# Performance work log

Hardware: AMD Instinct MI355X
Metric: run time of the kernel (lower is better)

The kernel has to match this reference:

```python
import jax, jax.numpy as jnp
import numpy as np

NEG_INF = -1e9  # stands in for the -inf diagonal mask of criss-cross attention
BN_EPS = 1e-5


def conv1x1(x, w, b=None):
    # x: [B,Cin,H,W], w: [Cout,Cin]
    y = jnp.einsum('bchw,oc->bohw', x, w)
    if b is not None:
        y = y + b[None, :, None, None]
    return y


def criss_cross(qf, kf, vf, q_w, q_b, k_w, k_b, v_w, v_b, gamma):
    # Criss-cross attention (CCNet): row + column affinity, joint softmax, aggregate.
    B, C, H, W = vf.shape
    q = conv1x1(qf, q_w, q_b)  # [B,Ci,H,W]
    k = conv1x1(kf, k_w, k_b)  # [B,Ci,H,W]
    v = conv1x1(vf, v_w, v_b)  # [B,C,H,W]
    # column-wise (along H) energy, with -inf on the self position (h == h')
    eH = jnp.einsum('bchw,bcHw->bhwH', q, k)
    eH = eH + NEG_INF * jnp.eye(H, dtype=eH.dtype)[:, None, :]  # [H,1,H] broadcasts over w
    # row-wise (along W) energy
    eW = jnp.einsum('bchw,bchW->bhwW', q, k)
    att = jax.nn.softmax(jnp.concatenate([eH, eW], axis=-1), axis=-1)  # [B,H,W,H+W]
    aH, aW = att[..., :H], att[..., H:]
    outH = jnp.einsum('bcHw,bhwH->bchw', v, aH)
    outW = jnp.einsum('bchW,bhwW->bchw', v, aW)
    return gamma * (outH + outW) + vf


def batchnorm(x, scale, bias):
    # training-mode BN over (N,H,W)
    mean = x.mean(axis=(0, 2, 3), keepdims=True)
    var = x.var(axis=(0, 2, 3), keepdims=True)
    xh = (x - mean) * jax.lax.rsqrt(var + BN_EPS)
    return xh * scale[None, :, None, None] + bias[None, :, None, None]


def setup_inputs() -> dict:
    key = jax.random.key(0)
    ks = jax.random.split(key, 16)
    B, C, H, W = 8, 512, 96, 96
    Hh, Wh = 48, 48
    Cin = C // 2    # 256
    Ci = C // 16    # 32
    s = 0.02
    inp = {
        'low_feature': jax.random.normal(ks[0], (B, C, H, W), jnp.float32),
        'high_feature': jax.random.normal(ks[1], (B, C, Hh, Wh), jnp.float32),
        'conv1_w': jax.random.normal(ks[2], (Cin, C), jnp.float32) * s,
        'conv1_b': jnp.zeros((Cin,), jnp.float32),
        'conv2_w': jax.random.normal(ks[3], (Cin, C), jnp.float32) * s,
        'conv2_b': jnp.zeros((Cin,), jnp.float32),
        'q_w': jax.random.normal(ks[4], (Ci, Cin), jnp.float32) * s,
        'q_b': jnp.zeros((Ci,), jnp.float32),
        'k_w': jax.random.normal(ks[5], (Ci, Cin), jnp.float32) * s,
        'k_b': jnp.zeros((Ci,), jnp.float32),
        'v_w': jax.random.normal(ks[6], (Cin, Cin), jnp.float32) * s,
        'v_b': jnp.zeros((Cin,), jnp.float32),
        'gamma': jnp.array(0.1, jnp.float32),
        'bottleneck_w': jax.random.normal(ks[7], (C, Cin + C), jnp.float32) * s,
        'bn_scale': jnp.ones((C,), jnp.float32),
        'bn_bias': jnp.zeros((C,), jnp.float32),
    }
    return inp


def reference(low_feature, high_feature, conv1_w, conv1_b, conv2_w, conv2_b,
              q_w, q_b, k_w, k_b, v_w, v_b, gamma, bottleneck_w, bn_scale, bn_bias):
    B, C, H, W = low_feature.shape
    hf = jax.image.resize(high_feature, (B, high_feature.shape[1], H, W), method='bilinear')
    qf = conv1x1(low_feature, conv1_w, conv1_b)   # [B,C/2,H,W]
    vf = conv1x1(hf, conv2_w, conv2_b)            # [B,C/2,H,W]
    for _ in range(2):  # module applies the same attention twice
        vf = criss_cross(qf, vf, vf, q_w, q_b, k_w, k_b, v_w, v_b, gamma)
    cat = jnp.concatenate([vf, hf], axis=1)       # [B, C/2 + C, H, W]
    out = conv1x1(cat, bottleneck_w)              # bias=False
    out = batchnorm(out, bn_scale, bn_bias)
    return jax.nn.relu(out)
```

## Files before the change

kernel.cpp:

```cpp
#include <hip/hip_runtime.h>
#include <hip/hip_bf16.h>

typedef __hip_bfloat16 bf16;
typedef __attribute__((ext_vector_type(8))) short short8;
typedef __attribute__((ext_vector_type(4))) float f32x4;

constexpr int kHW = 96 * 96;

__device__ __forceinline__ float b2f(bf16 x){ return __bfloat162float(x); }
__device__ __forceinline__ bf16  f2b(float x){ return __float2bfloat16(x); }
__device__ __forceinline__ unsigned short b2u(bf16 x){ return *(unsigned short*)&x; }

#define SW(r, g) ((r)*32 + ((((g) ^ (((r) >> 1) & 3))) << 3))


__global__ void k_zero(float* __restrict__ p){
  int i = blockIdx.x*256 + threadIdx.x;
  if (i < 1024) p[i] = 0.0f;
}

__global__ void k_cvt(const float* __restrict__ s, bf16* __restrict__ d, int n){
  int i = blockIdx.x*256 + threadIdx.x;
  if (i < n) d[i] = f2b(s[i]);
}

__global__ __launch_bounds__(256) void k_upsample(const float* __restrict__ hi,
                                                  bf16* __restrict__ hf_t){
  int y = blockIdx.x, b = blockIdx.y, t = threadIdx.x;
  int j = y >> 1;
  int j0, j1; float wy0, wy1;
  if ((y & 1) == 0){ j0 = j - 1; if (j0 < 0) j0 = 0; j1 = j; wy0 = 0.25f; wy1 = 0.75f; }
  else             { j0 = j; j1 = j + 1; if (j1 > 47) j1 = 47; wy0 = 0.75f; wy1 = 0.25f; }
  __shared__ __align__(16) float sm[2][128][49];
  for (int c0 = 0; c0 < 512; c0 += 128){
    for (int e = t; e < 2*128*48; e += 256){
      int cl = e / 96; int r = e % 96; int jj = r / 48; int i = r % 48;
      int row = jj ? j1 : j0;
      sm[jj][cl][i] = hi[(((size_t)b*512 + c0 + cl)*48 + row)*48 + i];
    }
    __syncthreads();
    for (int e = t; e < 96*128; e += 256){
      int x = e >> 7; int cl = e & 127;
      int i = x >> 1; int i0, i1; float wx0, wx1;
      if ((x & 1) == 0){ i0 = i - 1; if (i0 < 0) i0 = 0; i1 = i; wx0 = 0.25f; wx1 = 0.75f; }
      else             { i0 = i; i1 = i + 1; if (i1 > 47) i1 = 47; wx0 = 0.75f; wx1 = 0.25f; }
      float v = wy0*(wx0*sm[0][cl][i0] + wx1*sm[0][cl][i1])
              + wy1*(wx0*sm[1][cl][i0] + wx1*sm[1][cl][i1]);
      hf_t[(((size_t)b*96 + x)*96 + y)*512 + c0 + cl] = f2b(v);
    }
    __syncthreads();
  }
}

__global__ void k_qqw(const float* __restrict__ q_w, const float* __restrict__ c1_w,
                      bf16* __restrict__ qq_wb){
  int gid = blockIdx.x*256 + threadIdx.x;
  int o = gid >> 9, c = gid & 511;
  float acc = 0.f;
  for (int k = 0; k < 256; k++) acc += q_w[o*256 + k] * c1_w[k*512 + c];
  qq_wb[gid] = f2b(acc);
}
__global__ void k_qqb(const float* __restrict__ q_w, const float* __restrict__ c1_b,
                      const float* __restrict__ q_b, float* __restrict__ qq_b){
  int o = threadIdx.x; if (o >= 32) return;
  float acc = q_b[o];
  for (int k = 0; k < 256; k++) acc += q_w[o*256 + k] * c1_b[k];
  qq_b[o] = acc;
}

__global__ __launch_bounds__(256) void k_mfma_gemm(const bf16* __restrict__ A,
                                                   const bf16* __restrict__ Wb,
                                                   const float* __restrict__ bias,
                                                   bf16* __restrict__ out,
                                                   int K, int O){
  int b = blockIdx.z, n0 = blockIdx.x*128, o0 = blockIdx.y*128;
  int t = threadIdx.x, lane = t & 63, wv = t >> 6;
  int m_off = (wv & 1)*64, o_off = (wv >> 1)*64;
  int lm = lane & 15, lk = lane >> 4;
  __shared__ __align__(16) bf16 As[2][128*32];
  __shared__ __align__(16) bf16 Ws[2][128*32];
  f32x4 acc[4][4] = {};
  const bf16* Ab = A + (size_t)b*kHW*K;
  int nl0 = t >> 2, gp = t & 3, p0 = gp*8;
  uint4 pa0, pa1, pw0, pw1;
  pa0 = *(const uint4*)&Ab[(size_t)(n0+nl0)*K + p0];
  pa1 = *(const uint4*)&Ab[(size_t)(n0+nl0+64)*K + p0];
  pw0 = *(const uint4*)&Wb[(size_t)(o0+nl0)*K + p0];
  pw1 = *(const uint4*)&Wb[(size_t)(o0+nl0+64)*K + p0];
  *(uint4*)&As[0][SW(nl0, gp)]    = pa0;
  *(uint4*)&As[0][SW(nl0+64, gp)] = pa1;
  *(uint4*)&Ws[0][SW(nl0, gp)]    = pw0;
  *(uint4*)&Ws[0][SW(nl0+64, gp)] = pw1;
  int cur = 0;
  int NS = K >> 5;
  for (int s = 0; s < NS; s++){
    if (s+1 < NS){
      int c0 = (s+1)*32;
      pa0 = *(const uint4*)&Ab[(size_t)(n0+nl0)*K + c0 + p0];
      pa1 = *(const uint4*)&Ab[(size_t)(n0+nl0+64)*K + c0 + p0];
      pw0 = *(const uint4*)&Wb[(size_t)(o0+nl0)*K + c0 + p0];
      pw1 = *(const uint4*)&Wb[(size_t)(o0+nl0+64)*K + c0 + p0];
    }
    __syncthreads();
    short8 af[4], bfr[4];
    #pragma unroll
    for (int i = 0; i < 4; i++){
      af[i]  = *(const short8*)&As[cur][SW(m_off + i*16 + lm, lk)];
      bfr[i] = *(const short8*)&Ws[cur][SW(o_off + i*16 + lm, lk)];
    }
    #pragma unroll
    for (int i = 0; i < 4; i++)
      #pragma unroll
      for (int j = 0; j < 4; j++)
        acc[i][j] = __builtin_amdgcn_mfma_f32_16x16x32_bf16(af[i], bfr[j], acc[i][j], 0, 0, 0);
    if (s+1 < NS){
      int nx = cur ^ 1;
      *(uint4*)&As[nx][SW(nl0, gp)]    = pa0;
      *(uint4*)&As[nx][SW(nl0+64, gp)] = pa1;
      *(uint4*)&Ws[nx][SW(nl0, gp)]    = pw0;
      *(uint4*)&Ws[nx][SW(nl0+64, gp)] = pw1;
      cur = nx;
    }
  }
  #pragma unroll
  for (int j = 0; j < 4; j++){
    int oc = o0 + o_off + j*16 + lm;
    float bs = bias ? bias[oc] : 0.0f;
    #pragma unroll
    for (int i = 0; i < 4; i++){
      int rbase = n0 + m_off + i*16 + lk*4;
      #pragma unroll
      for (int r = 0; r < 4; r++)
        out[((size_t)b*kHW + rbase + r)*(size_t)O + oc] = f2b(acc[i][j][r] + bs);
    }
  }
}

__global__ __launch_bounds__(256) void k_bneck_mfma(const bf16* __restrict__ vf,
                                                    const bf16* __restrict__ hf,
                                                    const bf16* __restrict__ Wb,
                                                    bf16* __restrict__ out,
                                                    float* __restrict__ s1,
                                                    float* __restrict__ s2){
  int b = blockIdx.z, n0 = blockIdx.x*128, o0 = blockIdx.y*128;
  int t = threadIdx.x, lane = t & 63, wv = t >> 6;
  int m_off = (wv & 1)*64, o_off = (wv >> 1)*64;
  int lm = lane & 15, lk = lane >> 4;
  __shared__ __align__(16) bf16 As[2][128*32];
  __shared__ __align__(16) bf16 Ws[2][128*32];
  __shared__ float l1[128];
  __shared__ float l2[128];
  if (t < 128){ l1[t] = 0.f; l2[t] = 0.f; }
  f32x4 acc[4][4] = {};
  int nl0 = t >> 2, gp = t & 3, p0 = gp*8;
  const bf16* vfb = vf + (size_t)b*kHW*256;
  const bf16* hfb = hf + (size_t)b*kHW*512;
  uint4 pa0, pa1, pw0, pw1;
  pa0 = *(const uint4*)&vfb[(size_t)(n0+nl0)*256 + p0];
  pa1 = *(const uint4*)&vfb[(size_t)(n0+nl0+64)*256 + p0];
  pw0 = *(const uint4*)&Wb[(size_t)(o0+nl0)*768 + p0];
  pw1 = *(const uint4*)&Wb[(size_t)(o0+nl0+64)*768 + p0];
  *(uint4*)&As[0][SW(nl0, gp)]    = pa0;
  *(uint4*)&As[0][SW(nl0+64, gp)] = pa1;
  *(uint4*)&Ws[0][SW(nl0, gp)]    = pw0;
  *(uint4*)&Ws[0][SW(nl0+64, gp)] = pw1;
  int cur = 0;
  for (int s = 0; s < 24; s++){
    if (s+1 < 24){
      int c0 = (s+1)*32;
      if (c0 < 256){
        pa0 = *(const uint4*)&vfb[(size_t)(n0+nl0)*256 + c0 + p0];
        pa1 = *(const uint4*)&vfb[(size_t)(n0+nl0+64)*256 + c0 + p0];
      } else {
        int cc = c0 - 256;
        pa0 = *(const uint4*)&hfb[(size_t)(n0+nl0)*512 + cc + p0];
        pa1 = *(const uint4*)&hfb[(size_t)(n0+nl0+64)*512 + cc + p0];
      }
      pw0 = *(const uint4*)&Wb[(size_t)(o0+nl0)*768 + c0 + p0];
      pw1 = *(const uint4*)&Wb[(size_t)(o0+nl0+64)*768 + c0 + p0];
    }
    __syncthreads();
    short8 af[4], bfr[4];
    #pragma unroll
    for (int i = 0; i < 4; i++){
      af[i]  = *(const short8*)&As[cur][SW(m_off + i*16 + lm, lk)];
      bfr[i] = *(const short8*)&Ws[cur][SW(o_off + i*16 + lm, lk)];
    }
    #pragma unroll
    for (int i = 0; i < 4; i++)
      #pragma unroll
      for (int j = 0; j < 4; j++)
        acc[i][j] = __builtin_amdgcn_mfma_f32_16x16x32_bf16(af[i], bfr[j], acc[i][j], 0, 0, 0);
    if (s+1 < 24){
      int nx = cur ^ 1;
      *(uint4*)&As[nx][SW(nl0, gp)]    = pa0;
      *(uint4*)&As[nx][SW(nl0+64, gp)] = pa1;
      *(uint4*)&Ws[nx][SW(nl0, gp)]    = pw0;
      *(uint4*)&Ws[nx][SW(nl0+64, gp)] = pw1;
      cur = nx;
    }
  }
  #pragma unroll
  for (int j = 0; j < 4; j++){
    int oc = o0 + o_off + j*16 + lm;
    float p1 = 0.f, p2 = 0.f;
    #pragma unroll
    for (int i = 0; i < 4; i++){
      int rbase = n0 + m_off + i*16 + lk*4;
      #pragma unroll
      for (int r = 0; r < 4; r++){
        float v = acc[i][j][r];
        p1 += v; p2 += v*v;
        out[((size_t)b*kHW + rbase + r)*512 + oc] = f2b(v);
      }
    }
    int cl = o_off + j*16 + lm;
    atomicAdd(&l1[cl], p1);
    atomicAdd(&l2[cl], p2);
  }
  __syncthreads();
  if (t < 128){
    atomicAdd(&s1[o0 + t], l1[t]);
    atomicAdd(&s2[o0 + t], l2[t]);
  }
}

__global__ __launch_bounds__(256) void k_qmfma(const float* __restrict__ low,
                                               const bf16* __restrict__ qq_wb,
                                               const float* __restrict__ qq_b,
                                               bf16* __restrict__ q_t){
  int n0 = blockIdx.x*64, b = blockIdx.y, t = threadIdx.x;
  int lane = t & 63, wv = t >> 6;
  int m_off = wv*16;
  int lm = lane & 15, lk = lane >> 4;
  __shared__ __align__(16) bf16 As[64*36];
  __shared__ __align__(16) bf16 Ws[32*40];
  f32x4 acc[2] = {};
  const float* low_b = low + (size_t)b*512*kHW;
  int c2 = (t & 15)*2;
  int xg = t >> 4;
  for (int c0 = 0; c0 < 512; c0 += 32){
    const float* p0 = low_b + (size_t)(c0 + c2)*kHW + n0 + xg*4;
    float4 a0 = *(const float4*)p0;
    float4 a1 = *(const float4*)(p0 + kHW);
    float f0[4] = {a0.x, a0.y, a0.z, a0.w};
    float f1[4] = {a1.x, a1.y, a1.z, a1.w};
    #pragma unroll
    for (int u = 0; u < 4; u++){
      ushort2 pr;
      bf16 v0 = f2b(f0[u]), v1 = f2b(f1[u]);
      pr.x = b2u(v0); pr.y = b2u(v1);
      *(ushort2*)&As[(xg*4 + u)*36 + c2] = pr;
    }
    if (t < 128){
      int ol = t >> 2, p = t & 3;
      *(uint4*)&Ws[ol*40 + p*8] = *(const uint4*)&qq_wb[(size_t)ol*512 + c0 + p*8];
    }
    __syncthreads();
    short8 af = *(const short8*)&As[(m_off + lm)*36 + lk*8];
    short8 b0 = *(const short8*)&Ws[lm*40 + lk*8];
    short8 b1 = *(const short8*)&Ws[(16 + lm)*40 + lk*8];
    acc[0] = __builtin_amdgcn_mfma_f32_16x16x32_bf16(af, b0, acc[0], 0, 0, 0);
    acc[1] = __builtin_amdgcn_mfma_f32_16x16x32_bf16(af, b1, acc[1], 0, 0, 0);
    __syncthreads();
  }
  #pragma unroll
  for (int j = 0; j < 2; j++){
    int oc = j*16 + lm;
    float bs = qq_b[oc];
    #pragma unroll
    for (int r = 0; r < 4; r++){
      int ng = n0 + m_off + lk*4 + r;
      int h = ng / 96, x = ng - h*96;
      q_t[(((size_t)b*96 + x)*96 + h)*32 + oc] = f2b(acc[j][r] + bs);
    }
  }
}

__global__ __launch_bounds__(256) void k_kmfma(const bf16* __restrict__ A,
                                               const bf16* __restrict__ Wk,
                                               const float* __restrict__ bias,
                                               bf16* __restrict__ out){
  int n0 = blockIdx.x*128, b = blockIdx.y;
  int t = threadIdx.x, lane = t & 63, wv = t >> 6;
  int m_off = wv*32;
  int lm = lane & 15, lk = lane >> 4;
  __shared__ __align__(16) bf16 As[2][128*32];
  __shared__ __align__(16) bf16 Ws[2][32*32];
  f32x4 acc[2][2] = {};
  const bf16* Ab = A + (size_t)b*kHW*256;
  int nl0 = t >> 2, gp = t & 3, p0 = gp*8;
  int ol = t >> 2;
  uint4 pa0, pa1, pw;
  pa0 = *(const uint4*)&Ab[(size_t)(n0+nl0)*256 + p0];
  pa1 = *(const uint4*)&Ab[(size_t)(n0+nl0+64)*256 + p0];
  if (t < 128) pw = *(const uint4*)&Wk[(size_t)ol*256 + p0];
  *(uint4*)&As[0][SW(nl0, gp)]    = pa0;
  *(uint4*)&As[0][SW(nl0+64, gp)] = pa1;
  if (t < 128) *(uint4*)&Ws[0][SW(ol, gp)] = pw;
  int cur = 0;
  for (int s = 0; s < 8; s++){
    if (s+1 < 8){
      int c0 = (s+1)*32;
      pa0 = *(const uint4*)&Ab[(size_t)(n0+nl0)*256 + c0 + p0];
      pa1 = *(const uint4*)&Ab[(size_t)(n0+nl0+64)*256 + c0 + p0];
      if (t < 128) pw = *(const uint4*)&Wk[(size_t)ol*256 + c0 + p0];
    }
    __syncthreads();
    short8 af[2], bfr[2];
    #pragma unroll
    for (int i = 0; i < 2; i++)
      af[i] = *(const short8*)&As[cur][SW(m_off + i*16 + lm, lk)];
    #pragma unroll
    for (int j = 0; j < 2; j++)
      bfr[j] = *(const short8*)&Ws[cur][SW(j*16 + lm, lk)];
    #pragma unroll
    for (int i = 0; i < 2; i++)
      #pragma unroll
      for (int j = 0; j < 2; j++)
        acc[i][j] = __builtin_amdgcn_mfma_f32_16x16x32_bf16(af[i], bfr[j], acc[i][j], 0, 0, 0);
    if (s+1 < 8){
      int nx = cur ^ 1;
      *(uint4*)&As[nx][SW(nl0, gp)]    = pa0;
      *(uint4*)&As[nx][SW(nl0+64, gp)] = pa1;
      if (t < 128) *(uint4*)&Ws[nx][SW(ol, gp)] = pw;
      cur = nx;
    }
  }
  #pragma unroll
  for (int j = 0; j < 2; j++){
    int oc = j*16 + lm;
    float bs = bias[oc];
    #pragma unroll
    for (int i = 0; i < 2; i++){
      int rbase = n0 + m_off + i*16 + lk*4;
      #pragma unroll
      for (int r = 0; r < 4; r++)
        out[((size_t)b*kHW + rbase + r)*32 + oc] = f2b(acc[i][j][r] + bs);
    }
  }
}

__global__ __launch_bounds__(256) void k_eH(const bf16* __restrict__ q_t,
                                            const bf16* __restrict__ k_t,
                                            bf16* __restrict__ att){
  int w = blockIdx.x, b = blockIdx.y, t = threadIdx.x;
  __shared__ float Qs[96][33];
  __shared__ float Ks[96][33];
  const bf16* Qp = q_t + (((size_t)b*96 + w)*96)*32;
  const bf16* Kp = k_t + (((size_t)b*96 + w)*96)*32;
  for (int e = t; e < 3072; e += 256){ Qs[e>>5][e&31] = b2f(Qp[e]); Ks[e>>5][e&31] = b2f(Kp[e]); }
  __syncthreads();
  int tj = t % 16, th = t / 16;
  float acc[6][6] = {};
  #pragma unroll 4
  for (int c = 0; c < 32; c++){
    float qa[6], kb[6];
    #pragma unroll
    for (int i = 0; i < 6; i++) qa[i] = Qs[th*6 + i][c];
    #pragma unroll
    for (int jj = 0; jj < 6; jj++) kb[jj] = Ks[tj*6 + jj][c];
    #pragma unroll
    for (int i = 0; i < 6; i++)
      #pragma unroll
      for (int jj = 0; jj < 6; jj++) acc[i][jj] += qa[i]*kb[jj];
  }
  #pragma unroll
  for (int i = 0; i < 6; i++){
    int h = th*6 + i;
    size_t base = (((size_t)b*96 + h)*96 + w)*192;
    #pragma unroll
    for (int jj = 0; jj < 6; jj++){
      int jg = tj*6 + jj;
      float e = acc[i][jj];
      if (jg == h) e += -1000000000.0f;
      att[base + jg] = f2b(e);
    }
  }
}

__global__ __launch_bounds__(256) void k_eW(const bf16* __restrict__ q_t,
                                            const bf16* __restrict__ k_t,
                                            bf16* __restrict__ att){
  int h = blockIdx.x, b = blockIdx.y, t = threadIdx.x;
  __shared__ float Qs[96][33];
  __shared__ float Ks[96][33];
  for (int e = t; e < 3072; e += 256){
    int wl = e >> 5, c = e & 31;
    size_t idx = (((size_t)b*96 + wl)*96 + h)*32 + c;
    Qs[wl][c] = b2f(q_t[idx]);
    Ks[wl][c] = b2f(k_t[idx]);
  }
  __syncthreads();
  int tj = t % 16, tw = t / 16;
  float acc[6][6] = {};
  #pragma unroll 4
  for (int c = 0; c < 32; c++){
    float qa[6], kb[6];
    #pragma unroll
    for (int i = 0; i < 6; i++) qa[i] = Qs[tw*6 + i][c];
    #pragma unroll
    for (int jj = 0; jj < 6; jj++) kb[jj] = Ks[tj*6 + jj][c];
    #pragma unroll
    for (int i = 0; i < 6; i++)
      #pragma unroll
      for (int jj = 0; jj < 6; jj++) acc[i][jj] += qa[i]*kb[jj];
  }
  #pragma unroll
  for (int i = 0; i < 6; i++){
    int wl = tw*6 + i;
    size_t base = (((size_t)b*96 + h)*96 + wl)*192 + 96;
    #pragma unroll
    for (int jj = 0; jj < 6; jj++) att[base + tj*6 + jj] = f2b(acc[i][jj]);
  }
}

__global__ __launch_bounds__(256) void k_softmax(bf16* __restrict__ att){
  int t = threadIdx.x;
  int row = blockIdx.x*4 + (t >> 6);
  int lane = t & 63;
  size_t base = (size_t)row * 192;
  float x0 = b2f(att[base + lane]);
  float x1 = b2f(att[base + 64 + lane]);
  float x2 = b2f(att[base + 128 + lane]);
  float m = fmaxf(x0, fmaxf(x1, x2));
  #pragma unroll
  for (int off = 32; off; off >>= 1) m = fmaxf(m, __shfl_xor(m, off));
  float e0 = __expf(x0 - m), e1 = __expf(x1 - m), e2 = __expf(x2 - m);
  float s = e0 + e1 + e2;
  #pragma unroll
  for (int off = 32; off; off >>= 1) s += __shfl_xor(s, off);
  float inv = 1.0f / s;
  att[base + lane]       = f2b(e0 * inv);
  att[base + 64 + lane]  = f2b(e1 * inv);
  att[base + 128 + lane] = f2b(e2 * inv);
}

__global__ __launch_bounds__(256) void k_outH_mfma(const bf16* __restrict__ att,
                                                   const bf16* __restrict__ v_t,
                                                   bf16* __restrict__ accb){
  int w = blockIdx.x, b = blockIdx.y, t = threadIdx.x;
  int lane = t & 63, wv = t >> 6;
  int m_off = (wv & 1)*48, o_off = (wv >> 1)*128;
  int lm = lane & 15, lk = lane >> 4;
  __shared__ __align__(16) bf16 As[96*36];
  __shared__ __align__(16) bf16 Vt[256*36];
  f32x4 acc[3][8] = {};
  const bf16* Vb = v_t + ((size_t)b*96 + w)*96*256;
  for (int j0 = 0; j0 < 96; j0 += 32){
    for (int e = t; e < 384; e += 256){
      int h = e >> 2, p = e & 3;
      *(uint4*)&As[h*36 + p*8] =
        *(const uint4*)&att[(((size_t)b*96 + h)*96 + w)*192 + j0 + p*8];
    }
    for (int e = t; e < 512; e += 256){
      int jj2 = (e & 15)*2, cg = e >> 4;
      const bf16* p = Vb + (size_t)(j0 + jj2)*256 + cg*8;
      uint4 a0 = *(const uint4*)p;
      uint4 a1 = *(const uint4*)(p + 256);
      const unsigned short* u0 = (const unsigned short*)&a0;
      const unsigned short* u1 = (const unsigned short*)&a1;
      #pragma unroll
      for (int u = 0; u < 8; u++){
        ushort2 pr; pr.x = u0[u]; pr.y = u1[u];
        *(ushort2*)&Vt[(cg*8 + u)*36 + jj2] = pr;
      }
    }
    __syncthreads();
    short8 af[3], bfr[8];
    #pragma unroll
    for (int i = 0; i < 3; i++)
      af[i] = *(const short8*)&As[(m_off + i*16 + lm)*36 + lk*8];
    #pragma unroll
    for (int j = 0; j < 8; j++)
      bfr[j] = *(const short8*)&Vt[(o_off + j*16 + lm)*36 + lk*8];
    #pragma unroll
    for (int i = 0; i < 3; i++)
      #pragma unroll
      for (int j = 0; j < 8; j++)
        acc[i][j] = __builtin_amdgcn_mfma_f32_16x16x32_bf16(af[i], bfr[j], acc[i][j], 0, 0, 0);
    __syncthreads();
  }
  #pragma unroll
  for (int j = 0; j < 8; j++){
    int c = o_off + j*16 + lm;
    #pragma unroll
    for (int i = 0; i < 3; i++){
      int hbase = m_off + i*16 + lk*4;
      #pragma unroll
      for (int r = 0; r < 4; r++)
        accb[(((size_t)b*96 + w)*96 + hbase + r)*256 + c] = f2b(acc[i][j][r]);
    }
  }
}

__global__ __launch_bounds__(256) void k_outW_mfma(const bf16* __restrict__ att,
                                                   const bf16* __restrict__ v_t,
                                                   const bf16* __restrict__ accb,
                                                   const float* __restrict__ gamma_p,
                                                   bf16* __restrict__ vf_t){
  int h = blockIdx.x, b = blockIdx.y, t = threadIdx.x;
  int lane = t & 63, wv = t >> 6;
  int m_off = (wv & 1)*48, o_off = (wv >> 1)*128;
  int lm = lane & 15, lk = lane >> 4;
  __shared__ __align__(16) bf16 As[96*36];
  __shared__ __align__(16) bf16 Vt[256*36];
  f32x4 acc[3][8] = {};
  for (int j0 = 0; j0 < 96; j0 += 32){
    for (int e = t; e < 384; e += 256){
      int wl = e >> 2, p = e & 3;
      *(uint4*)&As[wl*36 + p*8] =
        *(const uint4*)&att[(((size_t)b*96 + h)*96 + wl)*192 + 96 + j0 + p*8];
    }
    for (int e = t; e < 512; e += 256){
      int jj2 = (e & 15)*2, cg = e >> 4;
      const bf16* p = v_t + (((size_t)b*96 + j0 + jj2)*96 + h)*256 + cg*8;
      uint4 a0 = *(const uint4*)p;
      uint4 a1 = *(const uint4*)(p + 96*256);
      const unsigned short* u0 = (const unsigned short*)&a0;
      const unsigned short* u1 = (const unsigned short*)&a1;
      #pragma unroll
      for (int u = 0; u < 8; u++){
        ushort2 pr; pr.x = u0[u]; pr.y = u1[u];
        *(ushort2*)&Vt[(cg*8 + u)*36 + jj2] = pr;
      }
    }
    __syncthreads();
    short8 af[3], bfr[8];
    #pragma unroll
    for (int i = 0; i < 3; i++)
      af[i] = *(const short8*)&As[(m_off + i*16 + lm)*36 + lk*8];
    #pragma unroll
    for (int j = 0; j < 8; j++)
      bfr[j] = *(const short8*)&Vt[(o_off + j*16 + lm)*36 + lk*8];
    #pragma unroll
    for (int i = 0; i < 3; i++)
      #pragma unroll
      for (int j = 0; j < 8; j++)
        acc[i][j] = __builtin_amdgcn_mfma_f32_16x16x32_bf16(af[i], bfr[j], acc[i][j], 0, 0, 0);
    __syncthreads();
  }
  float g = gamma_p[0];
  #pragma unroll
  for (int j = 0; j < 8; j++){
    int c = o_off + j*16 + lm;
    #pragma unroll
    for (int i = 0; i < 3; i++){
      int wbase = m_off + i*16 + lk*4;
      #pragma unroll
      for (int r = 0; r < 4; r++){
        size_t idx = (((size_t)b*96 + wbase + r)*96 + h)*256 + c;
        vf_t[idx] = f2b(b2f(vf_t[idx]) + g*(acc[i][j][r] + b2f(accb[idx])));
      }
    }
  }
}

__global__ void k_bnprep(const float* __restrict__ s1, const float* __restrict__ s2,
                         const float* __restrict__ sc, const float* __restrict__ bi,
                         float2* __restrict__ ab){
  int co = blockIdx.x*256 + threadIdx.x;
  if (co >= 512) return;
  const float N = 73728.0f;
  float mean = s1[co] / N;
  float var  = s2[co] / N - mean*mean;
  if (var < 0.f) var = 0.f;
  float a = rsqrtf(var + 1e-5f) * sc[co];
  ab[co] = make_float2(a, bi[co] - mean*a);
}

__global__ __launch_bounds__(256) void k_bnout(const bf16* __restrict__ bt,
                                               const float2* __restrict__ ab,
                                               float* __restrict__ out){
  int w0 = blockIdx.x*32, h = blockIdx.y, b = blockIdx.z, t = threadIdx.x;
  __shared__ float Tl[32][33];
  for (int co0 = 0; co0 < 512; co0 += 32){
    for (int e = t; e < 1024; e += 256){
      int wl = e >> 5, co = e & 31;
      Tl[wl][co] = b2f(bt[(((size_t)b*96 + w0 + wl)*96 + h)*512 + co0 + co]);
    }
    __syncthreads();
    for (int e = t; e < 1024; e += 256){
      int co = e >> 5, wl = e & 31;
      float2 s = ab[co0 + co];
      float v = fmaxf(Tl[wl][co]*s.x + s.y, 0.0f);
      out[(((size_t)b*512 + co0 + co)*96 + h)*96 + w0 + wl] = v;
    }
    __syncthreads();
  }
}

extern "C" void kernel_launch(void* const* d_in, const int* in_sizes, int n_in,
                              void* d_out, int out_size, void* d_ws, size_t ws_size,
                              hipStream_t stream){
  (void)in_sizes; (void)n_in; (void)out_size; (void)ws_size;
  const float* low   = (const float*)d_in[0];
  const float* high  = (const float*)d_in[1];
  const float* c1w   = (const float*)d_in[2];
  const float* c1b   = (const float*)d_in[3];
  const float* c2w   = (const float*)d_in[4];
  const float* c2b   = (const float*)d_in[5];
  const float* qw    = (const float*)d_in[6];
  const float* qb    = (const float*)d_in[7];
  const float* kw    = (const float*)d_in[8];
  const float* kb    = (const float*)d_in[9];
  const float* vw    = (const float*)d_in[10];
  const float* vb    = (const float*)d_in[11];
  const float* gamma = (const float*)d_in[12];
  const float* bw    = (const float*)d_in[13];
  const float* bns   = (const float*)d_in[14];
  const float* bnb   = (const float*)d_in[15];
  float* out = (float*)d_out;

  char* wsb = (char*)d_ws;
  bf16*   hf_t = (bf16*) (wsb + 0);
  bf16*   vf_t = (bf16*) (wsb + 75497472);
  bf16*   q_t  = (bf16*) (wsb + 113246208);
  bf16*   qq_wb= (bf16*) (wsb + 117964800);
  bf16*   wk   = (bf16*) (wsb + 117997568);
  float*  qq_b = (float*)(wsb + 118030336);
  float*  s1   = (float*)(wsb + 118030464);
  float*  s2   = (float*)(wsb + 118032512);
  float2* ab   = (float2*)(wsb + 118034560);
  bf16*   wbb  = (bf16*) (wsb + 118038656);
  bf16*   wc2  = (bf16*) (wsb + 118825088);
  bf16*   wv   = (bf16*) (wsb + 119087232);
  bf16*   v_t  = (bf16*) (wsb + 119218304);
  bf16*   att  = (bf16*) (wsb + 156967040);
  bf16*   accb = (bf16*) (wsb + 185278592);
  bf16*   k_t  = (bf16*) (wsb + 185278592);
  bf16*   bt   = (bf16*) (wsb + 119218304);

  k_zero<<<4, 256, 0, stream>>>(s1);
  k_cvt<<<1536, 256, 0, stream>>>(bw,  wbb, 393216);
  k_cvt<<<512,  256, 0, stream>>>(c2w, wc2, 131072);
  k_cvt<<<256,  256, 0, stream>>>(vw,  wv,  65536);
  k_cvt<<<32,   256, 0, stream>>>(kw,  wk,  8192);
  k_upsample<<<dim3(96, 8), 256, 0, stream>>>(high, hf_t);
  k_qqw<<<64, 256, 0, stream>>>(qw, c1w, qq_wb);
  k_qqb<<<1, 64, 0, stream>>>(qw, c1b, qb, qq_b);
  k_mfma_gemm<<<dim3(72, 2, 8), 256, 0, stream>>>(hf_t, wc2, c2b, vf_t, 512, 256);
  k_qmfma<<<dim3(144, 8), 256, 0, stream>>>(low, qq_wb, qq_b, q_t);

  for (int r = 0; r < 2; r++){
    k_kmfma<<<dim3(72, 8), 256, 0, stream>>>(vf_t, wk, kb, k_t);
    k_mfma_gemm<<<dim3(72, 2, 8), 256, 0, stream>>>(vf_t, wv, vb, v_t, 256, 256);
    k_eH<<<dim3(96, 8), 256, 0, stream>>>(q_t, k_t, att);
    k_eW<<<dim3(96, 8), 256, 0, stream>>>(q_t, k_t, att);
    k_softmax<<<18432, 256, 0, stream>>>(att);
    k_outH_mfma<<<dim3(96, 8), 256, 0, stream>>>(att, v_t, accb);
    k_outW_mfma<<<dim3(96, 8), 256, 0, stream>>>(att, v_t, accb, gamma, vf_t);
  }

  k_bneck_mfma<<<dim3(72, 4, 8), 256, 0, stream>>>(vf_t, hf_t, wbb, bt, s1, s2);
  k_bnprep<<<2, 256, 0, stream>>>(s1, s2, bns, bnb, ab);
  k_bnout<<<dim3(3, 96, 8), 256, 0, stream>>>(bt, ab, out);
}
```

Before: 956.3 us.

## Replace softmax pass with row stats and apply normalization inside aggregation kernels

Instead of rewriting the full attention tensor with normalized probabilities, a new kernel computes only per-row max and inverse sum, and the outH/outW kernels apply exp and scaling while staging attention tiles into shared memory. The eH/eW loads and the BN output transpose are also vectorized with wider loads. This removes a full read-write pass over the attention buffer. In exchange it adds exp work to the aggregation kernels, and the fused path is only taken when the workspace is large enough to hold the stats buffer.

```diff
diff --git a/kernel.cpp b/kernel.cpp
--- a/kernel.cpp
+++ b/kernel.cpp
@@ -10,6 +10,7 @@
 __device__ __forceinline__ float b2f(bf16 x){ return __bfloat162float(x); }
 __device__ __forceinline__ bf16  f2b(float x){ return __float2bfloat16(x); }
 __device__ __forceinline__ unsigned short b2u(bf16 x){ return *(unsigned short*)&x; }
+__device__ __forceinline__ float s2f(short u){ return __uint_as_float(((unsigned)(unsigned short)u) << 16); }
 
 #define SW(r, g) ((r)*32 + ((((g) ^ (((r) >> 1) & 3))) << 3))
 
@@ -345,11 +346,23 @@
                                             const bf16* __restrict__ k_t,
                                             bf16* __restrict__ att){
   int w = blockIdx.x, b = blockIdx.y, t = threadIdx.x;
-  __shared__ float Qs[96][33];
-  __shared__ float Ks[96][33];
+  __shared__ __align__(16) float Qs[96][36];
+  __shared__ __align__(16) float Ks[96][36];
   const bf16* Qp = q_t + (((size_t)b*96 + w)*96)*32;
   const bf16* Kp = k_t + (((size_t)b*96 + w)*96)*32;
-  for (int e = t; e < 3072; e += 256){ Qs[e>>5][e&31] = b2f(Qp[e]); Ks[e>>5][e&31] = b2f(Kp[e]); }
+  for (int e = t; e < 384; e += 256){
+    int row = e >> 2, cg = (e & 3)*8;
+    short8 qv = *(const short8*)&Qp[row*32 + cg];
+    short8 kv = *(const short8*)&Kp[row*32 + cg];
+    float4 q0 = {s2f(qv[0]), s2f(qv[1]), s2f(qv[2]), s2f(qv[3])};
+    float4 q1 = {s2f(qv[4]), s2f(qv[5]), s2f(qv[6]), s2f(qv[7])};
+    float4 k0 = {s2f(kv[0]), s2f(kv[1]), s2f(kv[2]), s2f(kv[3])};
+    float4 k1 = {s2f(kv[4]), s2f(kv[5]), s2f(kv[6]), s2f(kv[7])};
+    *(float4*)&Qs[row][cg]     = q0;
+    *(float4*)&Qs[row][cg + 4] = q1;
+    *(float4*)&Ks[row][cg]     = k0;
+    *(float4*)&Ks[row][cg + 4] = k1;
+  }
   __syncthreads();
   int tj = t % 16, th = t / 16;
   float acc[6][6] = {};
@@ -383,13 +396,21 @@
                                             const bf16* __restrict__ k_t,
                                             bf16* __restrict__ att){
   int h = blockIdx.x, b = blockIdx.y, t = threadIdx.x;
-  __shared__ float Qs[96][33];
-  __shared__ float Ks[96][33];
-  for (int e = t; e < 3072; e += 256){
-    int wl = e >> 5, c = e & 31;
-    size_t idx = (((size_t)b*96 + wl)*96 + h)*32 + c;
-    Qs[wl][c] = b2f(q_t[idx]);
-    Ks[wl][c] = b2f(k_t[idx]);
+  __shared__ __align__(16) float Qs[96][36];
+  __shared__ __align__(16) float Ks[96][36];
+  for (int e = t; e < 384; e += 256){
+    int wl = e >> 2, cg = (e & 3)*8;
+    size_t idx = (((size_t)b*96 + wl)*96 + h)*32 + cg;
+    short8 qv = *(const short8*)&q_t[idx];
+    short8 kv = *(const short8*)&k_t[idx];
+    float4 q0 = {s2f(qv[0]), s2f(qv[1]), s2f(qv[2]), s2f(qv[3])};
+    float4 q1 = {s2f(qv[4]), s2f(qv[5]), s2f(qv[6]), s2f(qv[7])};
+    float4 k0 = {s2f(kv[0]), s2f(kv[1]), s2f(kv[2]), s2f(kv[3])};
+    float4 k1 = {s2f(kv[4]), s2f(kv[5]), s2f(kv[6]), s2f(kv[7])};
+    *(float4*)&Qs[wl][cg]     = q0;
+    *(float4*)&Qs[wl][cg + 4] = q1;
+    *(float4*)&Ks[wl][cg]     = k0;
+    *(float4*)&Ks[wl][cg + 4] = k1;
   }
   __syncthreads();
   int tj = t % 16, tw = t / 16;
@@ -436,8 +457,28 @@
   att[base + 128 + lane] = f2b(e2 * inv);
 }
 
+__global__ __launch_bounds__(256) void k_rowstat(const bf16* __restrict__ att,
+                                                 float2* __restrict__ rstat){
+  int t = threadIdx.x;
+  int row = blockIdx.x*4 + (t >> 6);
+  int lane = t & 63;
+  size_t base = (size_t)row * 192;
+  float x0 = b2f(att[base + lane]);
+  float x1 = b2f(att[base + 64 + lane]);
+  float x2 = b2f(att[base + 128 + lane]);
+  float m = fmaxf(x0, fmaxf(x1, x2));
+  #pragma unroll
+  for (int off = 32; off; off >>= 1) m = fmaxf(m, __shfl_xor(m, off));
+  float s = __expf(x0 - m) + __expf(x1 - m) + __expf(x2 - m);
+  #pragma unroll
+  for (int off = 32; off; off >>= 1) s += __shfl_xor(s, off);
+  if (lane == 0) rstat[row] = make_float2(m, 1.0f / s);
+}
+
+template<bool RS>
 __global__ __launch_bounds__(256) void k_outH_mfma(const bf16* __restrict__ att,
                                                    const bf16* __restrict__ v_t,
+                                                   const float2* __restrict__ rstat,
                                                    bf16* __restrict__ accb){
   int w = blockIdx.x, b = blockIdx.y, t = threadIdx.x;
   int lane = t & 63, wv = t >> 6;
@@ -445,13 +486,28 @@
   int lm = lane & 15, lk = lane >> 4;
   __shared__ __align__(16) bf16 As[96*36];
   __shared__ __align__(16) bf16 Vt[256*36];
+  __shared__ float2 Ls[96];
+  if (RS){
+    if (t < 96) Ls[t] = rstat[((size_t)b*96 + t)*96 + w];
+    __syncthreads();
+  }
   f32x4 acc[3][8] = {};
   const bf16* Vb = v_t + ((size_t)b*96 + w)*96*256;
   for (int j0 = 0; j0 < 96; j0 += 32){
     for (int e = t; e < 384; e += 256){
       int h = e >> 2, p = e & 3;
-      *(uint4*)&As[h*36 + p*8] =
-        *(const uint4*)&att[(((size_t)b*96 + h)*96 + w)*192 + j0 + p*8];
+      const bf16* src = &att[(((size_t)b*96 + h)*96 + w)*192 + j0 + p*8];
+      if (RS){
+        short8 rv = *(const short8*)src;
+        float2 st = Ls[h];
+        short8 ov;
+        #pragma unroll
+        for (int u = 0; u < 8; u++)
+          ov[u] = (short)b2u(f2b(__expf(s2f(rv[u]) - st.x) * st.y));
+        *(short8*)&As[h*36 + p*8] = ov;
+      } else {
+        *(uint4*)&As[h*36 + p*8] = *(const uint4*)src;
+      }
     }
     for (int e = t; e < 512; e += 256){
       int jj2 = (e & 15)*2, cg = e >> 4;
@@ -494,8 +550,10 @@
   }
 }
 
+template<bool RS>
 __global__ __launch_bounds__(256) void k_outW_mfma(const bf16* __restrict__ att,
                                                    const bf16* __restrict__ v_t,
+                                                   const float2* __restrict__ rstat,
                                                    const bf16* __restrict__ accb,
                                                    const float* __restrict__ gamma_p,
                                                    bf16* __restrict__ vf_t){
@@ -505,12 +563,27 @@
   int lm = lane & 15, lk = lane >> 4;
   __shared__ __align__(16) bf16 As[96*36];
   __shared__ __align__(16) bf16 Vt[256*36];
+  __shared__ float2 Ls[96];
+  if (RS){
+    if (t < 96) Ls[t] = rstat[((size_t)b*96 + h)*96 + t];
+    __syncthreads();
+  }
   f32x4 acc[3][8] = {};
   for (int j0 = 0; j0 < 96; j0 += 32){
     for (int e = t; e < 384; e += 256){
       int wl = e >> 2, p = e & 3;
-      *(uint4*)&As[wl*36 + p*8] =
-        *(const uint4*)&att[(((size_t)b*96 + h)*96 + wl)*192 + 96 + j0 + p*8];
+      const bf16* src = &att[(((size_t)b*96 + h)*96 + wl)*192 + 96 + j0 + p*8];
+      if (RS){
+        short8 rv = *(const short8*)src;
+        float2 st = Ls[wl];
+        short8 ov;
+        #pragma unroll
+        for (int u = 0; u < 8; u++)
+          ov[u] = (short)b2u(f2b(__expf(s2f(rv[u]) - st.x) * st.y));
+        *(short8*)&As[wl*36 + p*8] = ov;
+      } else {
+        *(uint4*)&As[wl*36 + p*8] = *(const uint4*)src;
+      }
     }
     for (int e = t; e < 512; e += 256){
       int jj2 = (e & 15)*2, cg = e >> 4;
@@ -573,14 +646,16 @@
                                                const float2* __restrict__ ab,
                                                float* __restrict__ out){
   int w0 = blockIdx.x*32, h = blockIdx.y, b = blockIdx.z, t = threadIdx.x;
-  __shared__ float Tl[32][33];
-  for (int co0 = 0; co0 < 512; co0 += 32){
-    for (int e = t; e < 1024; e += 256){
-      int wl = e >> 5, co = e & 31;
-      Tl[wl][co] = b2f(bt[(((size_t)b*96 + w0 + wl)*96 + h)*512 + co0 + co]);
-    }
-    __syncthreads();
-    for (int e = t; e < 1024; e += 256){
+  __shared__ float Tl[32][65];
+  int wl0 = t >> 3, cg0 = (t & 7)*8;
+  for (int co0 = 0; co0 < 512; co0 += 64){
+    uint4 d = *(const uint4*)&bt[(((size_t)b*96 + w0 + wl0)*96 + h)*512 + co0 + cg0];
+    const unsigned short* us = (const unsigned short*)&d;
+    #pragma unroll
+    for (int u = 0; u < 8; u++)
+      Tl[wl0][cg0 + u] = __uint_as_float(((unsigned)us[u]) << 16);
+    __syncthreads();
+    for (int e = t; e < 2048; e += 256){
       int co = e >> 5, wl = e & 31;
       float2 s = ab[co0 + co];
       float v = fmaxf(Tl[wl][co]*s.x + s.y, 0.0f);
@@ -593,7 +668,7 @@
 extern "C" void kernel_launch(void* const* d_in, const int* in_sizes, int n_in,
                               void* d_out, int out_size, void* d_ws, size_t ws_size,
                               hipStream_t stream){
-  (void)in_sizes; (void)n_in; (void)out_size; (void)ws_size;
+  (void)in_sizes; (void)n_in; (void)out_size;
   const float* low   = (const float*)d_in[0];
   const float* high  = (const float*)d_in[1];
   const float* c1w   = (const float*)d_in[2];
@@ -630,6 +705,9 @@
   bf16*   accb = (bf16*) (wsb + 185278592);
   bf16*   k_t  = (bf16*) (wsb + 185278592);
   bf16*   bt   = (bf16*) (wsb + 119218304);
+  const size_t RS_OFF = 223027328;
+  float2* rstat = (float2*)(wsb + RS_OFF);
+  bool have_rs = ws_size >= RS_OFF + 73728*sizeof(float2);
 
   k_zero<<<4, 256, 0, stream>>>(s1);
   k_cvt<<<1536, 256, 0, stream>>>(bw,  wbb, 393216);
@@ -647,9 +725,15 @@
     k_mfma_gemm<<<dim3(72, 2, 8), 256, 0, stream>>>(vf_t, wv, vb, v_t, 256, 256);
     k_eH<<<dim3(96, 8), 256, 0, stream>>>(q_t, k_t, att);
     k_eW<<<dim3(96, 8), 256, 0, stream>>>(q_t, k_t, att);
-    k_softmax<<<18432, 256, 0, stream>>>(att);
-    k_outH_mfma<<<dim3(96, 8), 256, 0, stream>>>(att, v_t, accb);
-    k_outW_mfma<<<dim3(96, 8), 256, 0, stream>>>(att, v_t, accb, gamma, vf_t);
+    if (have_rs){
+      k_rowstat<<<18432, 256, 0, stream>>>(att, rstat);
+      k_outH_mfma<true><<<dim3(96, 8), 256, 0, stream>>>(att, v_t, rstat, accb);
+      k_outW_mfma<true><<<dim3(96, 8), 256, 0, stream>>>(att, v_t, rstat, accb, gamma, vf_t);
+    } else {
+      k_softmax<<<18432, 256, 0, stream>>>(att);
+      k_outH_mfma<false><<<dim3(96, 8), 256, 0, stream>>>(att, v_t, nullptr, accb);
+      k_outW_mfma<false><<<dim3(96, 8), 256, 0, stream>>>(att, v_t, nullptr, accb, gamma, vf_t);
+    }
   }
 
   k_bneck_mfma<<<dim3(72, 4, 8), 256, 0, stream>>>(vf_t, hf_t, wbb, bt, s1, s2);
```

New measurement: 934.6 us. 1.02x faster.
